# Optimization experiments

Hardware: AMD Instinct MI355X
Metric: run time of the kernel (lower is better)

Reference implementation:

```python
import jax, jax.numpy as jnp
import numpy as np

SIGMA = 1.0  # isotropic Gaussian bandwidth (init kwarg)


def setup_inputs() -> dict:
    key = jax.random.key(0)
    X = jax.random.normal(key, (16384, 64), dtype=jnp.float32)
    return {"X": X}


def reference(X):
    # pairwise squared distances: ||x_i||^2 - 2 x_i.x_j + ||x_j||^2
    sumX2 = jnp.sum(X * X, axis=1, keepdims=True)          # [n, 1]
    D2 = sumX2 - 2.0 * (X @ X.T) + sumX2.T                  # [n, n]
    D2 = jnp.maximum(D2, 0.0)
    K = jnp.exp(-D2 / (2.0 * SIGMA ** 2))
    return K
```

## Files before the change

### kernel.cpp

```cpp
#include <hip/hip_runtime.h>
#include <stdint.h>


typedef __attribute__((ext_vector_type(8))) short  s16x8;
typedef __attribute__((ext_vector_type(4))) float  f32x4;
typedef __attribute__((ext_vector_type(4))) unsigned short u16x4;

#define DDIM 64
#define JT 8
#define LROW 36
#define LOG2E      1.4426950408889634f
#define HALF_LOG2E 0.7213475204444817f

__device__ inline unsigned short bf16_rne(float x) {
  uint32_t u = __builtin_bit_cast(uint32_t, x);
  uint32_t r = (u + 0x7fffu + ((u >> 16) & 1u));
  return (unsigned short)(r >> 16);
}
__device__ inline float bf16_to_f32(unsigned short h) {
  return __builtin_bit_cast(float, (uint32_t)h << 16);
}

__global__ __launch_bounds__(256) void k_cvt(const float* __restrict__ X,
                                             unsigned short* __restrict__ Xb) {
  int g = blockIdx.x * 256 + threadIdx.x;
  f32x4 v = reinterpret_cast<const f32x4*>(X)[g];
  u16x4 h;
  h[0] = bf16_rne(v[0]); h[1] = bf16_rne(v[1]);
  h[2] = bf16_rne(v[2]); h[3] = bf16_rne(v[3]);
  reinterpret_cast<u16x4*>(Xb)[g] = h;
}

__global__ __launch_bounds__(256) void k_norm(const unsigned short* __restrict__ Xb,
                                              float* __restrict__ nrm) {
  int row = blockIdx.x * 256 + threadIdx.x;
  const s16x8* p = reinterpret_cast<const s16x8*>(Xb + (size_t)row * DDIM);
  float s = 0.f;
#pragma unroll
  for (int k = 0; k < 8; ++k) {
    s16x8 h = p[k];
#pragma unroll
    for (int e = 0; e < 8; ++e) {
      float f = bf16_to_f32((unsigned short)h[e]);
      s += f * f;
    }
  }
  nrm[row] = -HALF_LOG2E * s;
}

__global__ __launch_bounds__(256, 3) void gauss_main(
    const unsigned short* __restrict__ Xb, const float* __restrict__ nrm,
    float* __restrict__ K, int n) {
  const int lane = threadIdx.x & 63;
  const int wid  = threadIdx.x >> 6;
  const int wr = wid >> 1;
  const int wc = wid & 1;
  const int l15 = lane & 15;
  const int lq  = lane >> 4;
  const int r8  = lane >> 3;
  const int e8  = lane & 7;

  __shared__ float tbuf[4][64 * LROW];
  float* buf = tbuf[wid];

  const int i0     = blockIdx.x * 128 + wr * 64;
  const int jstrip = blockIdx.y * (64 * JT);

  s16x8 a[4][2]; float hA[4];
#pragma unroll
  for (int mi = 0; mi < 4; ++mi) {
    const int row = i0 + mi * 16 + l15;
    a[mi][0] = *reinterpret_cast<const s16x8*>(Xb + (size_t)row * DDIM + lq * 8);
    a[mi][1] = *reinterpret_cast<const s16x8*>(Xb + (size_t)row * DDIM + 32 + lq * 8);
    hA[mi] = nrm[row];
  }

  s16x8 b[2][2][2];
  f32x4 hc[2][2];
#define ISSUE_B(slot, jt_)                                                     \
  do {                                                                         \
    const int j0_ = jstrip + (jt_) * 64 + wc * 32;                             \
    _Pragma("unroll") for (int ni = 0; ni < 2; ++ni) {                         \
      const int row_ = j0_ + ni * 16 + l15;                                    \
      b[slot][ni][0] = *reinterpret_cast<const s16x8*>(                        \
          Xb + (size_t)row_ * DDIM + lq * 8);                                  \
      b[slot][ni][1] = *reinterpret_cast<const s16x8*>(                        \
          Xb + (size_t)row_ * DDIM + 32 + lq * 8);                             \
      hc[slot][ni] = *reinterpret_cast<const f32x4*>(                          \
          nrm + j0_ + ni * 16 + lq * 4);                                       \
    }                                                                          \
  } while (0)

  ISSUE_B(0, 0);

#pragma unroll
  for (int jt = 0; jt < JT; ++jt) {
    const int slot = jt & 1;
    const int j0 = jstrip + jt * 64 + wc * 32;

    if (jt + 1 < JT) ISSUE_B(slot ^ 1, jt + 1);
    __builtin_amdgcn_sched_barrier(0x1 | 0x2 | 0x4 | 0x8);

    f32x4 acc[4][2] = {};
#pragma unroll
    for (int ks = 0; ks < 2; ++ks)
#pragma unroll
      for (int mi = 0; mi < 4; ++mi)
#pragma unroll
        for (int ni = 0; ni < 2; ++ni)
          acc[mi][ni] = __builtin_amdgcn_mfma_f32_16x16x32_bf16(
              b[slot][ni][ks], a[mi][ks], acc[mi][ni], 0, 0, 0);

    const bool diag = (i0 < j0 + 32) && (j0 < i0 + 64);

#pragma unroll
    for (int mi = 0; mi < 4; ++mi) {
      const int rg = i0 + mi * 16 + l15;
#pragma unroll
      for (int ni = 0; ni < 2; ++ni) {
        const int c0 = j0 + ni * 16 + lq * 4;
        f32x4 v;
        if (diag) {
#pragma unroll
          for (int r = 0; r < 4; ++r) {
            float e = exp2f(hA[mi] + hc[slot][ni][r] + LOG2E * acc[mi][ni][r]);
            v[r] = (rg == c0 + r) ? 1.0f : e;
          }
        } else {
#pragma unroll
          for (int r = 0; r < 4; ++r)
            v[r] = exp2f(hA[mi] + hc[slot][ni][r] + LOG2E * acc[mi][ni][r]);
        }
        *reinterpret_cast<f32x4*>(
            buf + (mi * 16 + l15) * LROW + ni * 16 + lq * 4) = v;
      }
    }

#pragma unroll
    for (int g = 0; g < 8; ++g) {
      const int row = g * 8 + r8;
      f32x4 t = *reinterpret_cast<const f32x4*>(buf + row * LROW + e8 * 4);
      *reinterpret_cast<f32x4*>(K + (size_t)(i0 + row) * n + j0 + e8 * 4) = t;
    }
  }
#undef ISSUE_B
}

__device__ inline short cvt1(float x, float& sq) {
  uint32_t u = __builtin_bit_cast(uint32_t, x);
  uint32_t r = (u + 0x7fffu + ((u >> 16) & 1u)) & 0xffff0000u;
  float hf = __builtin_bit_cast(float, r);
  sq += hf * hf;
  return (short)(r >> 16);
}
__device__ inline void issue_row(const float* __restrict__ X, int row, int lq,
                                 f32x4 r[4]) {
  const f32x4* p = reinterpret_cast<const f32x4*>(X + (size_t)row * DDIM + lq * 8);
  const f32x4* q = reinterpret_cast<const f32x4*>(X + (size_t)row * DDIM + 32 + lq * 8);
  r[0] = p[0]; r[1] = p[1]; r[2] = q[0]; r[3] = q[1];
}
__device__ inline void cvt_row(const f32x4 r[4], s16x8 h[2], float& hnorm) {
  float s = 0.f;
#pragma unroll
  for (int ks = 0; ks < 2; ++ks) {
    s16x8 hh;
    hh[0] = cvt1(r[2*ks][0], s);   hh[1] = cvt1(r[2*ks][1], s);
    hh[2] = cvt1(r[2*ks][2], s);   hh[3] = cvt1(r[2*ks][3], s);
    hh[4] = cvt1(r[2*ks+1][0], s); hh[5] = cvt1(r[2*ks+1][1], s);
    hh[6] = cvt1(r[2*ks+1][2], s); hh[7] = cvt1(r[2*ks+1][3], s);
    h[ks] = hh;
  }
  s += __shfl_xor(s, 16);
  s += __shfl_xor(s, 32);
  hnorm = -HALF_LOG2E * s;
}
__global__ __launch_bounds__(256, 2) void gauss_gram_kernel(
    const float* __restrict__ X, float* __restrict__ K, int n) {
  const int lane = threadIdx.x & 63;
  const int wid  = threadIdx.x >> 6;
  const int wr = wid >> 1, wc = wid & 1;
  const int l15 = lane & 15, lq = lane >> 4;
  const int e16 = lane & 15, r4 = lane >> 4;
  __shared__ float tbuf[4][64 * 68];
  float* buf = tbuf[wid];
  const int i0 = blockIdx.x * 128 + wr * 64;
  const int jstrip = blockIdx.y * (128 * JT);
  f32x4 araw[4][4];
#pragma unroll
  for (int mi = 0; mi < 4; ++mi) issue_row(X, i0 + mi * 16 + l15, lq, araw[mi]);
  f32x4 braw[4][4];
#pragma unroll
  for (int ni = 0; ni < 4; ++ni)
    issue_row(X, jstrip + wc * 64 + ni * 16 + l15, lq, braw[ni]);
  s16x8 a[4][2]; float hA[4];
#pragma unroll
  for (int mi = 0; mi < 4; ++mi) cvt_row(araw[mi], a[mi], hA[mi]);
#pragma unroll
  for (int jt = 0; jt < JT; ++jt) {
    const int j0 = jstrip + jt * 128 + wc * 64;
    s16x8 b[4][2]; float hcol[4][4];
#pragma unroll
    for (int ni = 0; ni < 4; ++ni) {
      float hB;
      cvt_row(braw[ni], b[ni], hB);
#pragma unroll
      for (int r = 0; r < 4; ++r) hcol[ni][r] = __shfl(hB, lq * 4 + r);
    }
    if (jt + 1 < JT) {
#pragma unroll
      for (int ni = 0; ni < 4; ++ni)
        issue_row(X, jstrip + (jt + 1) * 128 + wc * 64 + ni * 16 + l15, lq, braw[ni]);
    }
    __builtin_amdgcn_sched_barrier(0x1 | 0x2 | 0x4 | 0x8);
    f32x4 acc[4][4] = {};
#pragma unroll
    for (int ks = 0; ks < 2; ++ks)
#pragma unroll
      for (int mi = 0; mi < 4; ++mi)
#pragma unroll
        for (int ni = 0; ni < 4; ++ni)
          acc[mi][ni] = __builtin_amdgcn_mfma_f32_16x16x32_bf16(
              b[ni][ks], a[mi][ks], acc[mi][ni], 0, 0, 0);
#pragma unroll
    for (int mi = 0; mi < 4; ++mi) {
      const int rg = i0 + mi * 16 + l15;
#pragma unroll
      for (int ni = 0; ni < 4; ++ni) {
        const int c0 = j0 + ni * 16 + lq * 4;
        f32x4 v;
#pragma unroll
        for (int r = 0; r < 4; ++r) {
          float arg = fminf(hA[mi] + hcol[ni][r] + LOG2E * acc[mi][ni][r], 0.0f);
          float e = exp2f(arg);
          v[r] = (rg == c0 + r) ? 1.0f : e;
        }
        *reinterpret_cast<f32x4*>(buf + (mi * 16 + l15) * 68 + ni * 16 + lq * 4) = v;
      }
    }
#pragma unroll
    for (int g = 0; g < 16; ++g) {
      const int row = g * 4 + r4;
      f32x4 t = *reinterpret_cast<const f32x4*>(buf + row * 68 + e16 * 4);
      *reinterpret_cast<f32x4*>(K + (size_t)(i0 + row) * n + j0 + e16 * 4) = t;
    }
  }
}

extern "C" void kernel_launch(void* const* d_in, const int* in_sizes, int n_in,
                              void* d_out, int out_size, void* d_ws, size_t ws_size,
                              hipStream_t stream) {
  (void)n_in; (void)out_size;
  const float* X = (const float*)d_in[0];
  float* K = (float*)d_out;
  const int n = in_sizes[0] / DDIM;
  const size_t need = (size_t)n * DDIM * 2 + (size_t)n * 4;
  if (ws_size >= need) {
    unsigned short* Xb = (unsigned short*)d_ws;
    float* nrm = (float*)((char*)d_ws + (size_t)n * DDIM * 2);
    k_cvt<<<dim3(n * DDIM / 4 / 256), 256, 0, stream>>>(X, Xb);
    k_norm<<<dim3(n / 256), 256, 0, stream>>>(Xb, nrm);
    dim3 grid(n / 128, n / (64 * JT));
    gauss_main<<<grid, 256, 0, stream>>>(Xb, nrm, K, n);
  } else {
    dim3 grid(n / 128, n / (128 * JT));
    gauss_gram_kernel<<<grid, 256, 0, stream>>>(X, K, n);
  }
}
```

Measured before the change: 229.1 us.

## Restructure main kernel into row-sweep tiles with full-row coalesced stores

Replaces the 128x512 tile kernel with one that handles 16 rows across an 8192-column sweep. All four waves write into a shared, XOR-swizzled 16x512 buffer, then emit long contiguous row segments to K after a block barrier. It also deepens the B-operand prefetch to three slots. The aim is more sequential writes to the 1 GiB output, at the cost of block-wide barriers and less A-operand reuse per B load.

Result: slower. 334.6 us (+46.1%).

```diff
diff --git a/kernel.cpp b/kernel.cpp
--- a/kernel.cpp
+++ b/kernel.cpp
@@ -7,8 +7,7 @@
 typedef __attribute__((ext_vector_type(4))) unsigned short u16x4;
 
 #define DDIM 64
-#define JT 8
-#define LROW 36
+#define NT 16
 #define LOG2E      1.4426950408889634f
 #define HALF_LOG2E 0.7213475204444817f
 
@@ -48,102 +47,109 @@
   nrm[row] = -HALF_LOG2E * s;
 }
 
-__global__ __launch_bounds__(256, 3) void gauss_main(
+__global__ __launch_bounds__(256, 2) void gauss_sweep(
     const unsigned short* __restrict__ Xb, const float* __restrict__ nrm,
     float* __restrict__ K, int n) {
   const int lane = threadIdx.x & 63;
   const int wid  = threadIdx.x >> 6;
-  const int wr = wid >> 1;
-  const int wc = wid & 1;
-  const int l15 = lane & 15;
-  const int lq  = lane >> 4;
-  const int r8  = lane >> 3;
-  const int e8  = lane & 7;
-
-  __shared__ float tbuf[4][64 * LROW];
-  float* buf = tbuf[wid];
-
-  const int i0     = blockIdx.x * 128 + wr * 64;
-  const int jstrip = blockIdx.y * (64 * JT);
-
-  s16x8 a[4][2]; float hA[4];
-#pragma unroll
-  for (int mi = 0; mi < 4; ++mi) {
-    const int row = i0 + mi * 16 + l15;
-    a[mi][0] = *reinterpret_cast<const s16x8*>(Xb + (size_t)row * DDIM + lq * 8);
-    a[mi][1] = *reinterpret_cast<const s16x8*>(Xb + (size_t)row * DDIM + 32 + lq * 8);
-    hA[mi] = nrm[row];
-  }
-
-  s16x8 b[2][2][2];
-  f32x4 hc[2][2];
-#define ISSUE_B(slot, jt_)                                                     \
+  const int l15  = lane & 15;
+  const int lq   = lane >> 4;
+
+  __shared__ float sbuf[2][16 * 512];
+
+  const int i0    = blockIdx.x * 16;
+  const int jbase = blockIdx.y * 8192;
+
+  s16x8 a0 = *reinterpret_cast<const s16x8*>(Xb + (size_t)(i0 + l15) * DDIM + lq * 8);
+  s16x8 a1 = *reinterpret_cast<const s16x8*>(Xb + (size_t)(i0 + l15) * DDIM + 32 + lq * 8);
+  const float hA = nrm[i0 + l15];
+
+  s16x8 b[3][4][2];
+  f32x4 hc[3][4];
+#define SUBCOL(u) (jbase + ((u) >> 1) * 512 + wid * 128 + ((u) & 1) * 64)
+#define ISSUE(u)                                                               \
   do {                                                                         \
-    const int j0_ = jstrip + (jt_) * 64 + wc * 32;                             \
-    _Pragma("unroll") for (int ni = 0; ni < 2; ++ni) {                         \
-      const int row_ = j0_ + ni * 16 + l15;                                    \
-      b[slot][ni][0] = *reinterpret_cast<const s16x8*>(                        \
-          Xb + (size_t)row_ * DDIM + lq * 8);                                  \
-      b[slot][ni][1] = *reinterpret_cast<const s16x8*>(                        \
-          Xb + (size_t)row_ * DDIM + 32 + lq * 8);                             \
-      hc[slot][ni] = *reinterpret_cast<const f32x4*>(                          \
-          nrm + j0_ + ni * 16 + lq * 4);                                       \
+    const int slot_ = (u) % 3;                                                 \
+    const int jc_ = SUBCOL(u);                                                 \
+    _Pragma("unroll") for (int ni = 0; ni < 4; ++ni) {                         \
+      const size_t row_ = (size_t)(jc_ + ni * 16 + l15);                       \
+      b[slot_][ni][0] = *reinterpret_cast<const s16x8*>(                       \
+          Xb + row_ * DDIM + lq * 8);                                          \
+      b[slot_][ni][1] = *reinterpret_cast<const s16x8*>(                       \
+          Xb + row_ * DDIM + 32 + lq * 8);                                     \
+      hc[slot_][ni] = *reinterpret_cast<const f32x4*>(                         \
+          nrm + jc_ + ni * 16 + lq * 4);                                       \
     }                                                                          \
   } while (0)
 
-  ISSUE_B(0, 0);
-
-#pragma unroll
-  for (int jt = 0; jt < JT; ++jt) {
-    const int slot = jt & 1;
-    const int j0 = jstrip + jt * 64 + wc * 32;
-
-    if (jt + 1 < JT) ISSUE_B(slot ^ 1, jt + 1);
-    __builtin_amdgcn_sched_barrier(0x1 | 0x2 | 0x4 | 0x8);
-
-    f32x4 acc[4][2] = {};
-#pragma unroll
-    for (int ks = 0; ks < 2; ++ks)
-#pragma unroll
-      for (int mi = 0; mi < 4; ++mi)
-#pragma unroll
-        for (int ni = 0; ni < 2; ++ni)
-          acc[mi][ni] = __builtin_amdgcn_mfma_f32_16x16x32_bf16(
-              b[slot][ni][ks], a[mi][ks], acc[mi][ni], 0, 0, 0);
-
-    const bool diag = (i0 < j0 + 32) && (j0 < i0 + 64);
-
-#pragma unroll
-    for (int mi = 0; mi < 4; ++mi) {
-      const int rg = i0 + mi * 16 + l15;
-#pragma unroll
-      for (int ni = 0; ni < 2; ++ni) {
-        const int c0 = j0 + ni * 16 + lq * 4;
+  ISSUE(0);
+  ISSUE(1);
+
+#pragma unroll
+  for (int t = 0; t < NT; ++t) {
+    const int p = t & 1;
+
+#pragma unroll
+    for (int s = 0; s < 2; ++s) {
+      const int u = t * 2 + s;
+      const int slot = u % 3;
+      const int jc = SUBCOL(u);
+
+      if (u + 2 < 2 * NT) ISSUE(u + 2);
+      __builtin_amdgcn_sched_barrier(0x1 | 0x2 | 0x4 | 0x8);
+
+      f32x4 acc[4] = {};
+#pragma unroll
+      for (int ni = 0; ni < 4; ++ni)
+        acc[ni] = __builtin_amdgcn_mfma_f32_16x16x32_bf16(
+            b[slot][ni][0], a0, acc[ni], 0, 0, 0);
+#pragma unroll
+      for (int ni = 0; ni < 4; ++ni)
+        acc[ni] = __builtin_amdgcn_mfma_f32_16x16x32_bf16(
+            b[slot][ni][1], a1, acc[ni], 0, 0, 0);
+
+      const bool diag = (i0 < jc + 64) && (jc < i0 + 16);
+
+#pragma unroll
+      for (int ni = 0; ni < 4; ++ni) {
+        const int c0 = jc + ni * 16 + lq * 4;
         f32x4 v;
         if (diag) {
 #pragma unroll
           for (int r = 0; r < 4; ++r) {
-            float e = exp2f(hA[mi] + hc[slot][ni][r] + LOG2E * acc[mi][ni][r]);
-            v[r] = (rg == c0 + r) ? 1.0f : e;
+            float e = exp2f(hA + hc[slot][ni][r] + LOG2E * acc[ni][r]);
+            v[r] = (i0 + l15 == c0 + r) ? 1.0f : e;
           }
         } else {
 #pragma unroll
           for (int r = 0; r < 4; ++r)
-            v[r] = exp2f(hA[mi] + hc[slot][ni][r] + LOG2E * acc[mi][ni][r]);
+            v[r] = exp2f(hA + hc[slot][ni][r] + LOG2E * acc[ni][r]);
         }
-        *reinterpret_cast<f32x4*>(
-            buf + (mi * 16 + l15) * LROW + ni * 16 + lq * 4) = v;
+        const int chunk = wid * 32 + s * 16 + ni * 4 + lq;
+        const int pos = chunk ^ (l15 & 7);
+        *reinterpret_cast<f32x4*>(&sbuf[p][l15 * 512 + pos * 4]) = v;
       }
     }
 
-#pragma unroll
-    for (int g = 0; g < 8; ++g) {
-      const int row = g * 8 + r8;
-      f32x4 t = *reinterpret_cast<const f32x4*>(buf + row * LROW + e8 * 4);
-      *reinterpret_cast<f32x4*>(K + (size_t)(i0 + row) * n + j0 + e8 * 4) = t;
-    }
-  }
-#undef ISSUE_B
+    asm volatile("s_waitcnt lgkmcnt(0)" ::: "memory");
+    __builtin_amdgcn_s_barrier();
+    __builtin_amdgcn_sched_barrier(0);
+
+    const int jc0 = jbase + t * 512;
+#pragma unroll
+    for (int r = 0; r < 4; ++r) {
+      const int row = wid * 4 + r;
+#pragma unroll
+      for (int q = 0; q < 2; ++q) {
+        const int g = q * 64 + lane;
+        f32x4 v = *reinterpret_cast<const f32x4*>(
+            &sbuf[p][row * 512 + (g ^ (row & 7)) * 4]);
+        *reinterpret_cast<f32x4*>(K + (size_t)(i0 + row) * n + jc0 + g * 4) = v;
+      }
+    }
+  }
+#undef ISSUE
+#undef SUBCOL
 }
 
 __device__ inline short cvt1(float x, float& sq) {
@@ -184,7 +190,7 @@
   __shared__ float tbuf[4][64 * 68];
   float* buf = tbuf[wid];
   const int i0 = blockIdx.x * 128 + wr * 64;
-  const int jstrip = blockIdx.y * (128 * JT);
+  const int jstrip = blockIdx.y * (128 * 8);
   f32x4 araw[4][4];
 #pragma unroll
   for (int mi = 0; mi < 4; ++mi) issue_row(X, i0 + mi * 16 + l15, lq, araw[mi]);
@@ -196,7 +202,7 @@
 #pragma unroll
   for (int mi = 0; mi < 4; ++mi) cvt_row(araw[mi], a[mi], hA[mi]);
 #pragma unroll
-  for (int jt = 0; jt < JT; ++jt) {
+  for (int jt = 0; jt < 8; ++jt) {
     const int j0 = jstrip + jt * 128 + wc * 64;
     s16x8 b[4][2]; float hcol[4][4];
 #pragma unroll
@@ -206,7 +212,7 @@
 #pragma unroll
       for (int r = 0; r < 4; ++r) hcol[ni][r] = __shfl(hB, lq * 4 + r);
     }
-    if (jt + 1 < JT) {
+    if (jt + 1 < 8) {
 #pragma unroll
       for (int ni = 0; ni < 4; ++ni)
         issue_row(X, jstrip + (jt + 1) * 128 + wc * 64 + ni * 16 + l15, lq, braw[ni]);
@@ -259,10 +265,10 @@
     float* nrm = (float*)((char*)d_ws + (size_t)n * DDIM * 2);
     k_cvt<<<dim3(n * DDIM / 4 / 256), 256, 0, stream>>>(X, Xb);
     k_norm<<<dim3(n / 256), 256, 0, stream>>>(Xb, nrm);
-    dim3 grid(n / 128, n / (64 * JT));
-    gauss_main<<<grid, 256, 0, stream>>>(Xb, nrm, K, n);
+    dim3 grid(n / 16, n / 8192);
+    gauss_sweep<<<grid, 256, 0, stream>>>(Xb, nrm, K, n);
   } else {
-    dim3 grid(n / 128, n / (128 * JT));
+    dim3 grid(n / 128, n / (128 * 8));
     gauss_gram_kernel<<<grid, 256, 0, stream>>>(X, K, n);
   }
 }
```
